# Optimization experiments

Measured on AMD Instinct MI355X. Metric: run time of the kernel, lower is better.

## Reference

```python
import jax, jax.numpy as jnp
import numpy as np

OUT = 2048        # weight_size[0]
IN_BASE = 2048    # original input features
N_EMBED = 64      # replacements per iteration
IN_TOT = IN_BASE + 2 * N_EMBED  # 2176, weight_size[1]
NNZ_W = 400000
NNZ_B = 1024
BATCH = 8192


def setup_inputs() -> dict:
    key = jax.random.key(0)
    ks = jax.random.split(key, 10)
    return {
        "x": jax.random.normal(ks[0], (BATCH, IN_BASE), dtype=jnp.float32),
        "weight_vals": jax.random.normal(ks[1], (NNZ_W,), dtype=jnp.float32),
        "weight_rows": jax.random.randint(ks[2], (NNZ_W,), 0, OUT, dtype=jnp.int32),
        "weight_cols": jax.random.randint(ks[3], (NNZ_W,), 0, IN_TOT, dtype=jnp.int32),
        "bias_vals": jax.random.normal(ks[4], (NNZ_B,), dtype=jnp.float32),
        "bias_idx": jax.random.randint(ks[5], (NNZ_B,), 0, OUT, dtype=jnp.int32),
        "embed0_vals": jax.random.uniform(ks[6], (N_EMBED,), dtype=jnp.float32),
        "embed0_parents": jax.random.randint(ks[7], (N_EMBED,), 0, IN_BASE, dtype=jnp.int32),
        "embed1_vals": jax.random.uniform(ks[8], (N_EMBED,), dtype=jnp.float32),
        "embed1_parents": jax.random.randint(ks[9], (N_EMBED,), 0, IN_BASE + N_EMBED, dtype=jnp.int32),
    }


def reference(x, weight_vals, weight_rows, weight_cols, bias_vals, bias_idx,
              embed0_vals, embed0_parents, embed1_vals, embed1_parents):
    # EmbedLinear layers: each appends one new feature per stored row,
    # new_feat[:, c] = value[c] * x[:, parent[c]]  (single nnz per sparse row)
    x = jnp.concatenate([x, x[:, embed0_parents] * embed0_vals[None, :]], axis=1)  # [B, 2112]
    x = jnp.concatenate([x, x[:, embed1_parents] * embed1_vals[None, :]], axis=1)  # [B, 2176]
    # sparse weight -> dense via scatter-add (coalesce semantics sum duplicates)
    W = jnp.zeros((OUT, IN_TOT), dtype=weight_vals.dtype).at[weight_rows, weight_cols].add(weight_vals)
    b = jnp.zeros((OUT,), dtype=bias_vals.dtype).at[bias_idx].add(bias_vals)
    # (W @ x^T)^T + b  ==  x @ W^T + b
    return x @ W.T + b[None, :]
```

## Files before the change

kernel.cpp:

```cpp
#include <hip/hip_runtime.h>
#include <stdint.h>

#define OUT_F   2048
#define IN_BASE 2048
#define N_EMB   64
#define IN_TOT  2176
#define NNZ_W   400000
#define NNZ_B   1024
#define BATCH   8192

typedef __bf16 bf16x8 __attribute__((ext_vector_type(8)));
typedef __bf16 bf16x4 __attribute__((ext_vector_type(4)));
typedef float  floatx16 __attribute__((ext_vector_type(16)));

#define AS1 __attribute__((address_space(1)))
#define AS3 __attribute__((address_space(3)))

#define NSEG     391
#define SEG_NNZ  1024
#define CAP      24
#define NBIN     256
#define BIN_ELEMS (8 * IN_TOT)

#define NB_SCAT  NSEG
#define NB_BIAS  2
#define NB_BUILD BATCH

__global__ void __launch_bounds__(512) prep_kernel(
    const float* __restrict__ x,
    const float* __restrict__ e0v, const int* __restrict__ e0p,
    const float* __restrict__ e1v, const int* __restrict__ e1p,
    __bf16* __restrict__ xb,
    const float* __restrict__ wv, const int* __restrict__ wr,
    const int* __restrict__ wc,
    const float* __restrict__ bv, const int* __restrict__ bi,
    float* __restrict__ segv, unsigned short* __restrict__ segm,
    unsigned char* __restrict__ segc,
    float* __restrict__ bfp)
{
    const int tid = threadIdx.x;
    const int blk = blockIdx.x;

    if (blk < NB_SCAT) {
        __shared__ unsigned int hist[NBIN];
        if (tid < NBIN) hist[tid] = 0;
        __syncthreads();
#pragma unroll
        for (int r = 0; r < 2; r++) {
            const int i = blk * SEG_NNZ + r * 512 + tid;
            if (i < NNZ_W) {
                const int row = wr[i], col = wc[i];
                const int bin = row >> 3;
                const unsigned int rank = atomicAdd(&hist[bin], 1u);
                if (rank < CAP) {
                    const int p = (blk * NBIN + bin) * CAP + (int)rank;
                    segv[p] = wv[i];
                    segm[p] = (unsigned short)((row & 7) * IN_TOT + col);
                }
            }
        }
        __syncthreads();
        if (tid < NBIN)
            segc[blk * NBIN + tid] =
                (unsigned char)(hist[tid] < CAP ? hist[tid] : CAP);
    } else if (blk < NB_SCAT + NB_BIAS) {
        const int i = (blk - NB_SCAT) * 512 + tid;
        if (i < NNZ_B) unsafeAtomicAdd(bfp + bi[i], bv[i]);
    } else {
        const int b = blk - NB_SCAT - NB_BIAS;
        const float* xr = x + (size_t)b * IN_BASE;
        __bf16* xo = xb + (size_t)b * IN_TOT;

        {
            const float4 t = *(const float4*)(xr + tid * 4);
            bf16x4 o;
            o[0] = (__bf16)t.x; o[1] = (__bf16)t.y;
            o[2] = (__bf16)t.z; o[3] = (__bf16)t.w;
            *(bf16x4*)(xo + tid * 4) = o;
        }
        if (tid < 32) {
            const int g = 512 + tid;
            float v[4];
            if (g < 528) {
                const int j = (g - 512) * 4;
#pragma unroll
                for (int t = 0; t < 4; t++) v[t] = e0v[j + t] * xr[e0p[j + t]];
            } else {
                const int j = (g - 528) * 4;
#pragma unroll
                for (int t = 0; t < 4; t++) {
                    const int p = e1p[j + t];
                    const float base = (p < IN_BASE)
                        ? xr[p]
                        : e0v[p - IN_BASE] * xr[e0p[p - IN_BASE]];
                    v[t] = e1v[j + t] * base;
                }
            }
            bf16x4 o;
            o[0] = (__bf16)v[0]; o[1] = (__bf16)v[1];
            o[2] = (__bf16)v[2]; o[3] = (__bf16)v[3];
            *(bf16x4*)(xo + g * 4) = o;
        }
    }
}

__global__ void __launch_bounds__(512) accum_kernel(
    const float* __restrict__ segv, const unsigned short* __restrict__ segm,
    const unsigned char* __restrict__ segc,
    __bf16* __restrict__ Wb)
{
    __shared__ float Ws[BIN_ELEMS];
    const int tid = threadIdx.x;
    const int b   = blockIdx.x;

    for (int e = tid; e < BIN_ELEMS; e += 512) Ws[e] = 0.f;
    __syncthreads();

    for (int s = tid; s < NSEG; s += 512) {
        const int c    = segc[s * NBIN + b];
        const int base = (s * NBIN + b) * CAP;
        for (int j = 0; j < c; j++)
            atomicAdd(&Ws[segm[base + j]], segv[base + j]);
    }
    __syncthreads();

    __bf16* wo = Wb + (size_t)b * BIN_ELEMS;
    for (int e = tid; e < BIN_ELEMS / 4; e += 512) {
        bf16x4 o;
        o[0] = (__bf16)Ws[e * 4 + 0]; o[1] = (__bf16)Ws[e * 4 + 1];
        o[2] = (__bf16)Ws[e * 4 + 2]; o[3] = (__bf16)Ws[e * 4 + 3];
        *(bf16x4*)(wo + e * 4) = o;
    }
}

#define BM 256
#define BN 256
#define BK 64
#define NKT (IN_TOT / BK)
static_assert(NKT % 2 == 0, "pipeline consumes K-tiles in pairs");

#define CFENCE asm volatile("" ::: "memory")
#define BAR do { CFENCE; __builtin_amdgcn_s_barrier(); CFENCE; } while (0)
#define VMW(n) asm volatile("s_waitcnt vmcnt(" #n ")" ::: "memory")
#define NOPS do {} while (0)

#define STAGE(G, SBC, buf, tile, half) do {                                     \
    const __bf16* _s = (G) + (size_t)((half) * 128) * IN_TOT + (tile) * 64;     \
    char* _d = (SBC) + (buf) * 32768 + (half) * 16384 + tid * 16;               \
    __builtin_amdgcn_global_load_lds((AS1 void*)(uintptr_t)_s,                  \
                                     (AS3 void*)_d, 16, 0, 0);                  \
    __builtin_amdgcn_global_load_lds((AS1 void*)(uintptr_t)(_s + (size_t)64 * IN_TOT), \
                                     (AS3 void*)(_d + 8192), 16, 0, 0);         \
} while (0)

#define RD_A(pA, mq) do {                                                       \
    _Pragma("unroll") for (int ks = 0; ks < 4; ks++) {                          \
        const int kc = ks * 2 + khalf;                                          \
        _Pragma("unroll") for (int mi = 0; mi < 2; mi++) {                      \
            const int r = (mq) * 128 + wm * 64 + mi * 32 + l32;                 \
            a[mi * 4 + ks] = *(const bf16x8*)((pA) + r * 64 + ((kc ^ (r & 7)) * 8)); \
        }                                                                       \
    }                                                                           \
} while (0)

#define RD_B(pB, nq, barr) do {                                                 \
    _Pragma("unroll") for (int ks = 0; ks < 4; ks++) {                          \
        const int kc = ks * 2 + khalf;                                          \
        const int rb = (nq) * 128 + wn * 32 + l32;                              \
        barr[ks] = *(const bf16x8*)((pB) + rb * 64 + ((kc ^ (rb & 7)) * 8));    \
    }                                                                           \
} while (0)

#define MMPH(mq, nq, barr) do {                                                 \
    BAR;                                                                        \
    __builtin_amdgcn_s_setprio(1);                                              \
    _Pragma("unroll") for (int mi = 0; mi < 2; mi++)                            \
        _Pragma("unroll") for (int ks = 0; ks < 4; ks++)                        \
            acc[mq][mi][nq] = __builtin_amdgcn_mfma_f32_32x32x16_bf16(          \
                a[mi * 4 + ks], barr[ks], acc[mq][mi][nq], 0, 0, 0);            \
    __builtin_amdgcn_s_setprio(0);                                              \
    BAR;                                                                        \
} while (0)

#define KTILE(buf, STG1, STG2, STG3, STG4, W4) do {                             \
    const __bf16* _pA = sA + (buf) * 16384;                                     \
    const __bf16* _pB = sB + (buf) * 16384;                                     \
    RD_A(_pA, 0); RD_B(_pB, 0, b0);                                             \
    STG1;              MMPH(0, 0, b0);                                          \
    RD_B(_pB, 1, b1);                                                           \
    STG2;              MMPH(0, 1, b1);                                          \
    RD_A(_pA, 1);                                                               \
    STG3;              MMPH(1, 1, b1);                                          \
    STG4; W4;          MMPH(1, 0, b0);                                          \
} while (0)

__global__ void __launch_bounds__(512, 2) gemm_kernel(
    const __bf16* __restrict__ A,
    const __bf16* __restrict__ W,
    const float*  __restrict__ bias,
    float* __restrict__ C)
{
    __shared__ __align__(16) __bf16 sA[2 * 256 * 64];
    __shared__ __align__(16) __bf16 sB[2 * 256 * 64];

    const int tid   = threadIdx.x;
    const int bm    = blockIdx.x;
    const int bn    = blockIdx.y;
    const int wave  = tid >> 6;
    const int lane  = tid & 63;
    const int wm    = wave >> 2;
    const int wn    = wave & 3;
    const int l32   = lane & 31;
    const int khalf = lane >> 5;

    floatx16 acc[2][2][2] = {};
    bf16x8 a[8];
    bf16x8 b0[4], b1[4];

    const int srow   = tid >> 3;
    const int kchunk = ((tid & 7) ^ ((tid >> 3) & 7)) * 8;
    const __bf16* Ag = A + (size_t)(bm * BM + srow) * IN_TOT + kchunk;
    const __bf16* Wg = W + (size_t)(bn * BN + srow) * IN_TOT + kchunk;
    char* sAc = (char*)sA;
    char* sBc = (char*)sB;

    STAGE(Ag, sAc, 0, 0, 0);
    STAGE(Ag, sAc, 0, 0, 1);
    STAGE(Wg, sBc, 0, 0, 0);
    STAGE(Wg, sBc, 0, 0, 1);
    STAGE(Ag, sAc, 1, 1, 0);
    STAGE(Wg, sBc, 1, 1, 1);
    VMW(4);
    BAR;

#pragma unroll 1
    for (int i = 0; i < NKT / 2 - 1; ++i) {
        const int t1 = 2 * i + 1, t2 = 2 * i + 2, t3 = 2 * i + 3;
        KTILE(0, STAGE(Ag, sAc, 1, t1, 1), STAGE(Wg, sBc, 1, t1, 0),
                 STAGE(Ag, sAc, 0, t2, 0), STAGE(Wg, sBc, 0, t2, 1), VMW(4));
        KTILE(1, STAGE(Ag, sAc, 0, t2, 1), STAGE(Wg, sBc, 0, t2, 0),
                 STAGE(Ag, sAc, 1, t3, 0), STAGE(Wg, sBc, 1, t3, 1), VMW(4));
    }
    KTILE(0, STAGE(Ag, sAc, 1, NKT - 1, 1), STAGE(Wg, sBc, 1, NKT - 1, 0),
             NOPS, NOPS, VMW(0));
    KTILE(1, NOPS, NOPS, NOPS, NOPS, NOPS);

#pragma unroll
    for (int m = 0; m < 2; m++)
#pragma unroll
    for (int mi = 0; mi < 2; mi++)
#pragma unroll
    for (int n = 0; n < 2; n++) {
        const int colg = bn * BN + n * 128 + wn * 32 + l32;
        const float bvv = bias[colg];
        const int rowb = bm * BM + m * 128 + wm * 64 + mi * 32 + 4 * khalf;
#pragma unroll
        for (int reg = 0; reg < 16; reg++) {
            const int rowg = rowb + (reg & 3) + 8 * (reg >> 2);
            C[(size_t)rowg * OUT_F + colg] = acc[m][mi][n][reg] + bvv;
        }
    }
}

extern "C" void kernel_launch(void* const* d_in, const int* in_sizes, int n_in,
                              void* d_out, int out_size, void* d_ws, size_t ws_size,
                              hipStream_t stream) {
    const float* x      = (const float*)d_in[0];
    const float* w_vals = (const float*)d_in[1];
    const int*   w_rows = (const int*)  d_in[2];
    const int*   w_cols = (const int*)  d_in[3];
    const float* b_vals = (const float*)d_in[4];
    const int*   b_idx  = (const int*)  d_in[5];
    const float* e0v    = (const float*)d_in[6];
    const int*   e0p    = (const int*)  d_in[7];
    const float* e1v    = (const float*)d_in[8];
    const int*   e1p    = (const int*)  d_in[9];
    float* out = (float*)d_out;

    char* ws = (char*)d_ws;
    const size_t W_BF16_BYTES = (size_t)OUT_F * IN_TOT * 2;
    const size_t B_F32_BYTES  = (size_t)OUT_F * 4;
    const size_t XB_BYTES     = (size_t)BATCH * IN_TOT * 2;
    const size_t SEGV_BYTES   = (size_t)NSEG * NBIN * CAP * 4;
    const size_t SEGM_BYTES   = (size_t)NSEG * NBIN * CAP * 2;
    __bf16*         Wb   = (__bf16*)ws;
    float*          bfp  = (float*)(ws + W_BF16_BYTES);
    __bf16*         xb   = (__bf16*)(ws + W_BF16_BYTES + B_F32_BYTES);
    float*          segv = (float*)(ws + W_BF16_BYTES + B_F32_BYTES + XB_BYTES);
    unsigned short* segm = (unsigned short*)((char*)segv + SEGV_BYTES);
    unsigned char*  segc = (unsigned char*)((char*)segm + SEGM_BYTES);

    hipMemsetAsync(bfp, 0, B_F32_BYTES, stream);

    prep_kernel<<<NB_SCAT + NB_BIAS + NB_BUILD, 512, 0, stream>>>(
        x, e0v, e0p, e1v, e1p, xb,
        w_vals, w_rows, w_cols, b_vals, b_idx,
        segv, segm, segc, bfp);

    accum_kernel<<<NBIN, 512, 0, stream>>>(segv, segm, segc, Wb);

    dim3 grid(BATCH / BM, OUT_F / BN);
    gemm_kernel<<<grid, 512, 0, stream>>>(xb, Wb, bfp, out);
}
```

Measured before the change: 218.4 us.

## Fuse prep, accumulate and GEMM into one cooperative persistent kernel

Merges the three launches (scatter/convert prep, per-bin weight accumulation, bf16 MFMA GEMM) into a single cooperative kernel of 256 blocks separated by grid-wide syncs. Shared memory is a single 128 KB buffer reused across the phases. The goal is to remove the kernel launch gaps and tail effects between stages. In exchange, the prep phase runs on only 256 blocks with grid-stride loops instead of thousands of blocks. The GEMM launch shape is also pinned to exactly 256 tiles, and the grid syncs add their own cost.

```diff
diff --git a/kernel.cpp b/kernel.cpp
--- a/kernel.cpp
+++ b/kernel.cpp
@@ -1,5 +1,8 @@
 #include <hip/hip_runtime.h>
+#include <hip/hip_cooperative_groups.h>
 #include <stdint.h>
+
+namespace cg = cooperative_groups;
 
 #define OUT_F   2048
 #define IN_BASE 2048
@@ -21,117 +24,6 @@
 #define CAP      24
 #define NBIN     256
 #define BIN_ELEMS (8 * IN_TOT)
-
-#define NB_SCAT  NSEG
-#define NB_BIAS  2
-#define NB_BUILD BATCH
-
-__global__ void __launch_bounds__(512) prep_kernel(
-    const float* __restrict__ x,
-    const float* __restrict__ e0v, const int* __restrict__ e0p,
-    const float* __restrict__ e1v, const int* __restrict__ e1p,
-    __bf16* __restrict__ xb,
-    const float* __restrict__ wv, const int* __restrict__ wr,
-    const int* __restrict__ wc,
-    const float* __restrict__ bv, const int* __restrict__ bi,
-    float* __restrict__ segv, unsigned short* __restrict__ segm,
-    unsigned char* __restrict__ segc,
-    float* __restrict__ bfp)
-{
-    const int tid = threadIdx.x;
-    const int blk = blockIdx.x;
-
-    if (blk < NB_SCAT) {
-        __shared__ unsigned int hist[NBIN];
-        if (tid < NBIN) hist[tid] = 0;
-        __syncthreads();
-#pragma unroll
-        for (int r = 0; r < 2; r++) {
-            const int i = blk * SEG_NNZ + r * 512 + tid;
-            if (i < NNZ_W) {
-                const int row = wr[i], col = wc[i];
-                const int bin = row >> 3;
-                const unsigned int rank = atomicAdd(&hist[bin], 1u);
-                if (rank < CAP) {
-                    const int p = (blk * NBIN + bin) * CAP + (int)rank;
-                    segv[p] = wv[i];
-                    segm[p] = (unsigned short)((row & 7) * IN_TOT + col);
-                }
-            }
-        }
-        __syncthreads();
-        if (tid < NBIN)
-            segc[blk * NBIN + tid] =
-                (unsigned char)(hist[tid] < CAP ? hist[tid] : CAP);
-    } else if (blk < NB_SCAT + NB_BIAS) {
-        const int i = (blk - NB_SCAT) * 512 + tid;
-        if (i < NNZ_B) unsafeAtomicAdd(bfp + bi[i], bv[i]);
-    } else {
-        const int b = blk - NB_SCAT - NB_BIAS;
-        const float* xr = x + (size_t)b * IN_BASE;
-        __bf16* xo = xb + (size_t)b * IN_TOT;
-
-        {
-            const float4 t = *(const float4*)(xr + tid * 4);
-            bf16x4 o;
-            o[0] = (__bf16)t.x; o[1] = (__bf16)t.y;
-            o[2] = (__bf16)t.z; o[3] = (__bf16)t.w;
-            *(bf16x4*)(xo + tid * 4) = o;
-        }
-        if (tid < 32) {
-            const int g = 512 + tid;
-            float v[4];
-            if (g < 528) {
-                const int j = (g - 512) * 4;
-#pragma unroll
-                for (int t = 0; t < 4; t++) v[t] = e0v[j + t] * xr[e0p[j + t]];
-            } else {
-                const int j = (g - 528) * 4;
-#pragma unroll
-                for (int t = 0; t < 4; t++) {
-                    const int p = e1p[j + t];
-                    const float base = (p < IN_BASE)
-                        ? xr[p]
-                        : e0v[p - IN_BASE] * xr[e0p[p - IN_BASE]];
-                    v[t] = e1v[j + t] * base;
-                }
-            }
-            bf16x4 o;
-            o[0] = (__bf16)v[0]; o[1] = (__bf16)v[1];
-            o[2] = (__bf16)v[2]; o[3] = (__bf16)v[3];
-            *(bf16x4*)(xo + g * 4) = o;
-        }
-    }
-}
-
-__global__ void __launch_bounds__(512) accum_kernel(
-    const float* __restrict__ segv, const unsigned short* __restrict__ segm,
-    const unsigned char* __restrict__ segc,
-    __bf16* __restrict__ Wb)
-{
-    __shared__ float Ws[BIN_ELEMS];
-    const int tid = threadIdx.x;
-    const int b   = blockIdx.x;
-
-    for (int e = tid; e < BIN_ELEMS; e += 512) Ws[e] = 0.f;
-    __syncthreads();
-
-    for (int s = tid; s < NSEG; s += 512) {
-        const int c    = segc[s * NBIN + b];
-        const int base = (s * NBIN + b) * CAP;
-        for (int j = 0; j < c; j++)
-            atomicAdd(&Ws[segm[base + j]], segv[base + j]);
-    }
-    __syncthreads();
-
-    __bf16* wo = Wb + (size_t)b * BIN_ELEMS;
-    for (int e = tid; e < BIN_ELEMS / 4; e += 512) {
-        bf16x4 o;
-        o[0] = (__bf16)Ws[e * 4 + 0]; o[1] = (__bf16)Ws[e * 4 + 1];
-        o[2] = (__bf16)Ws[e * 4 + 2]; o[3] = (__bf16)Ws[e * 4 + 3];
-        *(bf16x4*)(wo + e * 4) = o;
-    }
-}
 
 #define BM 256
 #define BN 256
@@ -194,70 +86,177 @@
     STG4; W4;          MMPH(1, 0, b0);                                          \
 } while (0)
 
-__global__ void __launch_bounds__(512, 2) gemm_kernel(
-    const __bf16* __restrict__ A,
-    const __bf16* __restrict__ W,
-    const float*  __restrict__ bias,
+__global__ void __launch_bounds__(512, 2) fused_kernel(
+    const float* __restrict__ x,
+    const float* __restrict__ e0v, const int* __restrict__ e0p,
+    const float* __restrict__ e1v, const int* __restrict__ e1p,
+    const float* __restrict__ wv, const int* __restrict__ wr,
+    const int* __restrict__ wc,
+    const float* __restrict__ bv, const int* __restrict__ bi,
+    __bf16* __restrict__ xb,
+    float* __restrict__ segv, unsigned short* __restrict__ segm,
+    unsigned char* __restrict__ segc,
+    float* __restrict__ bfp,
+    __bf16* __restrict__ Wb,
     float* __restrict__ C)
 {
-    __shared__ __align__(16) __bf16 sA[2 * 256 * 64];
-    __shared__ __align__(16) __bf16 sB[2 * 256 * 64];
-
-    const int tid   = threadIdx.x;
-    const int bm    = blockIdx.x;
-    const int bn    = blockIdx.y;
-    const int wave  = tid >> 6;
-    const int lane  = tid & 63;
-    const int wm    = wave >> 2;
-    const int wn    = wave & 3;
-    const int l32   = lane & 31;
-    const int khalf = lane >> 5;
-
-    floatx16 acc[2][2][2] = {};
-    bf16x8 a[8];
-    bf16x8 b0[4], b1[4];
-
-    const int srow   = tid >> 3;
-    const int kchunk = ((tid & 7) ^ ((tid >> 3) & 7)) * 8;
-    const __bf16* Ag = A + (size_t)(bm * BM + srow) * IN_TOT + kchunk;
-    const __bf16* Wg = W + (size_t)(bn * BN + srow) * IN_TOT + kchunk;
-    char* sAc = (char*)sA;
-    char* sBc = (char*)sB;
-
-    STAGE(Ag, sAc, 0, 0, 0);
-    STAGE(Ag, sAc, 0, 0, 1);
-    STAGE(Wg, sBc, 0, 0, 0);
-    STAGE(Wg, sBc, 0, 0, 1);
-    STAGE(Ag, sAc, 1, 1, 0);
-    STAGE(Wg, sBc, 1, 1, 1);
-    VMW(4);
-    BAR;
+    __shared__ __align__(16) char smem[131072];
+    const int tid = threadIdx.x;
+    const int blk = blockIdx.x;
+    cg::grid_group grid = cg::this_grid();
+
+    {
+        unsigned int* hist = (unsigned int*)smem;
+        for (int s = blk; s < NSEG; s += 256) {
+            if (tid < NBIN) hist[tid] = 0;
+            __syncthreads();
+#pragma unroll
+            for (int r = 0; r < 2; r++) {
+                const int i = s * SEG_NNZ + r * 512 + tid;
+                if (i < NNZ_W) {
+                    const int row = wr[i], col = wc[i];
+                    const int bin = row >> 3;
+                    const unsigned int rank = atomicAdd(&hist[bin], 1u);
+                    if (rank < CAP) {
+                        const int p = (s * NBIN + bin) * CAP + (int)rank;
+                        segv[p] = wv[i];
+                        segm[p] = (unsigned short)((row & 7) * IN_TOT + col);
+                    }
+                }
+            }
+            __syncthreads();
+            if (tid < NBIN)
+                segc[s * NBIN + tid] =
+                    (unsigned char)(hist[tid] < CAP ? hist[tid] : CAP);
+            __syncthreads();
+        }
+
+        const int gbi = blk * 512 + tid;
+        if (gbi < NNZ_B) unsafeAtomicAdd(bfp + bi[gbi], bv[gbi]);
+
+        for (int b = blk; b < BATCH; b += 256) {
+            const float* xr = x + (size_t)b * IN_BASE;
+            __bf16* xo = xb + (size_t)b * IN_TOT;
+            {
+                const float4 t = *(const float4*)(xr + tid * 4);
+                bf16x4 o;
+                o[0] = (__bf16)t.x; o[1] = (__bf16)t.y;
+                o[2] = (__bf16)t.z; o[3] = (__bf16)t.w;
+                *(bf16x4*)(xo + tid * 4) = o;
+            }
+            if (tid < 32) {
+                const int g = 512 + tid;
+                float v[4];
+                if (g < 528) {
+                    const int j = (g - 512) * 4;
+#pragma unroll
+                    for (int t = 0; t < 4; t++) v[t] = e0v[j + t] * xr[e0p[j + t]];
+                } else {
+                    const int j = (g - 528) * 4;
+#pragma unroll
+                    for (int t = 0; t < 4; t++) {
+                        const int p = e1p[j + t];
+                        const float base = (p < IN_BASE)
+                            ? xr[p]
+                            : e0v[p - IN_BASE] * xr[e0p[p - IN_BASE]];
+                        v[t] = e1v[j + t] * base;
+                    }
+                }
+                bf16x4 o;
+                o[0] = (__bf16)v[0]; o[1] = (__bf16)v[1];
+                o[2] = (__bf16)v[2]; o[3] = (__bf16)v[3];
+                *(bf16x4*)(xo + g * 4) = o;
+            }
+        }
+    }
+    __threadfence();
+    grid.sync();
+
+    {
+        float* Ws = (float*)smem;
+        const int b = blk;
+        for (int e = tid; e < BIN_ELEMS; e += 512) Ws[e] = 0.f;
+        __syncthreads();
+        for (int s = tid; s < NSEG; s += 512) {
+            const int c    = segc[s * NBIN + b];
+            const int base = (s * NBIN + b) * CAP;
+            for (int j = 0; j < c; j++)
+                atomicAdd(&Ws[segm[base + j]], segv[base + j]);
+        }
+        __syncthreads();
+        __bf16* wo = Wb + (size_t)b * BIN_ELEMS;
+        for (int e = tid; e < BIN_ELEMS / 4; e += 512) {
+            bf16x4 o;
+            o[0] = (__bf16)Ws[e * 4 + 0]; o[1] = (__bf16)Ws[e * 4 + 1];
+            o[2] = (__bf16)Ws[e * 4 + 2]; o[3] = (__bf16)Ws[e * 4 + 3];
+            *(bf16x4*)(wo + e * 4) = o;
+        }
+    }
+    __threadfence();
+    grid.sync();
+
+    {
+        __bf16* sA = (__bf16*)smem;
+        __bf16* sB = (__bf16*)(smem + 65536);
+        const __bf16* A = xb;
+        const __bf16* W = Wb;
+        const float*  bias = bfp;
+
+        const int bm    = blk & 31;
+        const int bn    = blk >> 5;
+        const int wave  = tid >> 6;
+        const int lane  = tid & 63;
+        const int wm    = wave >> 2;
+        const int wn    = wave & 3;
+        const int l32   = lane & 31;
+        const int khalf = lane >> 5;
+
+        floatx16 acc[2][2][2] = {};
+        bf16x8 a[8];
+        bf16x8 b0[4], b1[4];
+
+        const int srow   = tid >> 3;
+        const int kchunk = ((tid & 7) ^ ((tid >> 3) & 7)) * 8;
+        const __bf16* Ag = A + (size_t)(bm * BM + srow) * IN_TOT + kchunk;
+        const __bf16* Wg = W + (size_t)(bn * BN + srow) * IN_TOT + kchunk;
+        char* sAc = (char*)sA;
+        char* sBc = (char*)sB;
+
+        STAGE(Ag, sAc, 0, 0, 0);
+        STAGE(Ag, sAc, 0, 0, 1);
+        STAGE(Wg, sBc, 0, 0, 0);
+        STAGE(Wg, sBc, 0, 0, 1);
+        STAGE(Ag, sAc, 1, 1, 0);
+        STAGE(Wg, sBc, 1, 1, 1);
+        VMW(4);
+        BAR;
 
 #pragma unroll 1
-    for (int i = 0; i < NKT / 2 - 1; ++i) {
-        const int t1 = 2 * i + 1, t2 = 2 * i + 2, t3 = 2 * i + 3;
-        KTILE(0, STAGE(Ag, sAc, 1, t1, 1), STAGE(Wg, sBc, 1, t1, 0),
-                 STAGE(Ag, sAc, 0, t2, 0), STAGE(Wg, sBc, 0, t2, 1), VMW(4));
-        KTILE(1, STAGE(Ag, sAc, 0, t2, 1), STAGE(Wg, sBc, 0, t2, 0),
-                 STAGE(Ag, sAc, 1, t3, 0), STAGE(Wg, sBc, 1, t3, 1), VMW(4));
-    }
-    KTILE(0, STAGE(Ag, sAc, 1, NKT - 1, 1), STAGE(Wg, sBc, 1, NKT - 1, 0),
-             NOPS, NOPS, VMW(0));
-    KTILE(1, NOPS, NOPS, NOPS, NOPS, NOPS);
-
-#pragma unroll
-    for (int m = 0; m < 2; m++)
-#pragma unroll
-    for (int mi = 0; mi < 2; mi++)
-#pragma unroll
-    for (int n = 0; n < 2; n++) {
-        const int colg = bn * BN + n * 128 + wn * 32 + l32;
-        const float bvv = bias[colg];
-        const int rowb = bm * BM + m * 128 + wm * 64 + mi * 32 + 4 * khalf;
-#pragma unroll
-        for (int reg = 0; reg < 16; reg++) {
-            const int rowg = rowb + (reg & 3) + 8 * (reg >> 2);
-            C[(size_t)rowg * OUT_F + colg] = acc[m][mi][n][reg] + bvv;
+        for (int i = 0; i < NKT / 2 - 1; ++i) {
+            const int t1 = 2 * i + 1, t2 = 2 * i + 2, t3 = 2 * i + 3;
+            KTILE(0, STAGE(Ag, sAc, 1, t1, 1), STAGE(Wg, sBc, 1, t1, 0),
+                     STAGE(Ag, sAc, 0, t2, 0), STAGE(Wg, sBc, 0, t2, 1), VMW(4));
+            KTILE(1, STAGE(Ag, sAc, 0, t2, 1), STAGE(Wg, sBc, 0, t2, 0),
+                     STAGE(Ag, sAc, 1, t3, 0), STAGE(Wg, sBc, 1, t3, 1), VMW(4));
+        }
+        KTILE(0, STAGE(Ag, sAc, 1, NKT - 1, 1), STAGE(Wg, sBc, 1, NKT - 1, 0),
+                 NOPS, NOPS, VMW(0));
+        KTILE(1, NOPS, NOPS, NOPS, NOPS, NOPS);
+
+#pragma unroll
+        for (int m = 0; m < 2; m++)
+#pragma unroll
+        for (int mi = 0; mi < 2; mi++)
+#pragma unroll
+        for (int n = 0; n < 2; n++) {
+            const int colg = bn * BN + n * 128 + wn * 32 + l32;
+            const float bvv = bias[colg];
+            const int rowb = bm * BM + m * 128 + wm * 64 + mi * 32 + 4 * khalf;
+#pragma unroll
+            for (int reg = 0; reg < 16; reg++) {
+                const int rowg = rowb + (reg & 3) + 8 * (reg >> 2);
+                C[(size_t)rowg * OUT_F + colg] = acc[m][mi][n][reg] + bvv;
+            }
         }
     }
 }
@@ -292,13 +291,13 @@
 
     hipMemsetAsync(bfp, 0, B_F32_BYTES, stream);
 
-    prep_kernel<<<NB_SCAT + NB_BIAS + NB_BUILD, 512, 0, stream>>>(
-        x, e0v, e0p, e1v, e1p, xb,
-        w_vals, w_rows, w_cols, b_vals, b_idx,
-        segv, segm, segc, bfp);
-
-    accum_kernel<<<NBIN, 512, 0, stream>>>(segv, segm, segc, Wb);
-
-    dim3 grid(BATCH / BM, OUT_F / BN);
-    gemm_kernel<<<grid, 512, 0, stream>>>(xb, Wb, bfp, out);
+    void* args[] = {
+        (void*)&x, (void*)&e0v, (void*)&e0p, (void*)&e1v, (void*)&e1p,
+        (void*)&w_vals, (void*)&w_rows, (void*)&w_cols,
+        (void*)&b_vals, (void*)&b_idx,
+        (void*)&xb, (void*)&segv, (void*)&segm, (void*)&segc,
+        (void*)&bfp, (void*)&Wb, (void*)&out
+    };
+    hipLaunchCooperativeKernel((const void*)fused_kernel,
+                               dim3(256), dim3(512), args, 0, stream);
 }
```

After: 493.6 us. +125.9%, slower.

## Replace interleaved phase pipeline with simple double-buffered stage/compute loop

Applied to the files above, without the earlier changes.

Drops the fine-grained schedule in which half-tile global-to-LDS loads were spread across four MFMA phases, each wrapped in barriers and s_setprio. Each K-tile now issues the whole next tile's loads up front, runs all LDS reads and MFMAs without barriers, then waits for all loads and syncs once. This removes most barriers and the priority toggling. In exchange it gives up the deliberate overlap between waves and the partial vmcnt waits, relying on two resident blocks per CU to hide memory latency.

```diff
diff --git a/kernel.cpp b/kernel.cpp
--- a/kernel.cpp
+++ b/kernel.cpp
@@ -137,7 +137,7 @@
 #define BN 256
 #define BK 64
 #define NKT (IN_TOT / BK)
-static_assert(NKT % 2 == 0, "pipeline consumes K-tiles in pairs");
+static_assert(NKT % 2 == 0, "loop consumes K-tiles in pairs");
 
 #define CFENCE asm volatile("" ::: "memory")
 #define BAR do { CFENCE; __builtin_amdgcn_s_barrier(); CFENCE; } while (0)
@@ -151,6 +151,13 @@
                                      (AS3 void*)_d, 16, 0, 0);                  \
     __builtin_amdgcn_global_load_lds((AS1 void*)(uintptr_t)(_s + (size_t)64 * IN_TOT), \
                                      (AS3 void*)(_d + 8192), 16, 0, 0);         \
+} while (0)
+
+#define STAGE_T(buf, tile) do {                                                 \
+    STAGE(Ag, sAc, buf, tile, 0);                                               \
+    STAGE(Ag, sAc, buf, tile, 1);                                               \
+    STAGE(Wg, sBc, buf, tile, 0);                                               \
+    STAGE(Wg, sBc, buf, tile, 1);                                               \
 } while (0)
 
 #define RD_A(pA, mq) do {                                                       \
@@ -171,27 +178,20 @@
     }                                                                           \
 } while (0)
 
-#define MMPH(mq, nq, barr) do {                                                 \
-    BAR;                                                                        \
-    __builtin_amdgcn_s_setprio(1);                                              \
+#define MMC(mq, nq, barr) do {                                                  \
     _Pragma("unroll") for (int mi = 0; mi < 2; mi++)                            \
         _Pragma("unroll") for (int ks = 0; ks < 4; ks++)                        \
             acc[mq][mi][nq] = __builtin_amdgcn_mfma_f32_32x32x16_bf16(          \
                 a[mi * 4 + ks], barr[ks], acc[mq][mi][nq], 0, 0, 0);            \
-    __builtin_amdgcn_s_setprio(0);                                              \
-    BAR;                                                                        \
-} while (0)
-
-#define KTILE(buf, STG1, STG2, STG3, STG4, W4) do {                             \
+} while (0)
+
+#define COMPUTE(buf) do {                                                       \
     const __bf16* _pA = sA + (buf) * 16384;                                     \
     const __bf16* _pB = sB + (buf) * 16384;                                     \
-    RD_A(_pA, 0); RD_B(_pB, 0, b0);                                             \
-    STG1;              MMPH(0, 0, b0);                                          \
-    RD_B(_pB, 1, b1);                                                           \
-    STG2;              MMPH(0, 1, b1);                                          \
+    RD_A(_pA, 0); RD_B(_pB, 0, b0); RD_B(_pB, 1, b1);                           \
+    MMC(0, 0, b0); MMC(0, 1, b1);                                               \
     RD_A(_pA, 1);                                                               \
-    STG3;              MMPH(1, 1, b1);                                          \
-    STG4; W4;          MMPH(1, 0, b0);                                          \
+    MMC(1, 1, b1); MMC(1, 0, b0);                                               \
 } while (0)
 
 __global__ void __launch_bounds__(512, 2) gemm_kernel(
@@ -224,26 +224,26 @@
     char* sAc = (char*)sA;
     char* sBc = (char*)sB;
 
-    STAGE(Ag, sAc, 0, 0, 0);
-    STAGE(Ag, sAc, 0, 0, 1);
-    STAGE(Wg, sBc, 0, 0, 0);
-    STAGE(Wg, sBc, 0, 0, 1);
-    STAGE(Ag, sAc, 1, 1, 0);
-    STAGE(Wg, sBc, 1, 1, 1);
-    VMW(4);
+    STAGE_T(0, 0);
+    VMW(0);
     BAR;
 
 #pragma unroll 1
     for (int i = 0; i < NKT / 2 - 1; ++i) {
-        const int t1 = 2 * i + 1, t2 = 2 * i + 2, t3 = 2 * i + 3;
-        KTILE(0, STAGE(Ag, sAc, 1, t1, 1), STAGE(Wg, sBc, 1, t1, 0),
-                 STAGE(Ag, sAc, 0, t2, 0), STAGE(Wg, sBc, 0, t2, 1), VMW(4));
-        KTILE(1, STAGE(Ag, sAc, 0, t2, 1), STAGE(Wg, sBc, 0, t2, 0),
-                 STAGE(Ag, sAc, 1, t3, 0), STAGE(Wg, sBc, 1, t3, 1), VMW(4));
-    }
-    KTILE(0, STAGE(Ag, sAc, 1, NKT - 1, 1), STAGE(Wg, sBc, 1, NKT - 1, 0),
-             NOPS, NOPS, VMW(0));
-    KTILE(1, NOPS, NOPS, NOPS, NOPS, NOPS);
+        STAGE_T(1, 2 * i + 1);
+        COMPUTE(0);
+        VMW(0);
+        BAR;
+        STAGE_T(0, 2 * i + 2);
+        COMPUTE(1);
+        VMW(0);
+        BAR;
+    }
+    STAGE_T(1, NKT - 1);
+    COMPUTE(0);
+    VMW(0);
+    BAR;
+    COMPUTE(1);
 
 #pragma unroll
     for (int m = 0; m < 2; m++)
```

After: 212.5 us. 2.7% less time.
